# Kernel optimization log

Measured on AMD Instinct MI355X. Metric: run time of the kernel, lower is better.

## Reference

```python
import jax, jax.numpy as jnp
import numpy as np

NUM_ROUTING = 3
EPS = 1e-8


def squash(s, axis=-1):
    # v = ||s||^2/(1+||s||^2) * s/||s||
    sq = jnp.sum(s * s, axis=axis, keepdims=True)
    return sq / (1.0 + sq) * s / (jnp.sqrt(sq) + EPS)


def setup_inputs() -> dict:
    key = jax.random.key(0)
    k1, k2 = jax.random.split(key)
    batch, in_caps, in_dim = 16, 2048, 64
    num_caps, dim_caps = 64, 32
    x = jax.random.normal(k1, (batch, in_caps, in_dim), dtype=jnp.float32)
    # learned transform W[j, d, k]  (torch shape (1,num_caps,1,dim_caps,in_dim) with singletons dropped)
    W = 0.01 * jax.random.normal(k2, (num_caps, dim_caps, in_dim), dtype=jnp.float32)
    return {"x": x, "W": W}


def reference(x, W):
    # u_hat[b,j,i,d] = sum_k W[j,d,k] * x[b,i,k]
    u_hat = jnp.einsum('jdk,bik->bjid', W, x)  # (b, num_caps, in_caps, dim_caps)
    u_hat_d = jax.lax.stop_gradient(u_hat)     # routing uses detached predictions

    b = jnp.zeros(u_hat.shape[:3] + (1,), dtype=u_hat.dtype)  # (b, J, I, 1)
    for _ in range(NUM_ROUTING - 1):
        c = jax.nn.softmax(b, axis=1)                # over output capsules J
        s = jnp.sum(c * u_hat_d, axis=2)             # (b, J, D)
        v = squash(s)
        # agreement uv[b,j,i] = <u_hat_d[b,j,i,:], v[b,j,:]>
        b = b + jnp.einsum('bjid,bjd->bji', u_hat_d, v)[..., None]

    c = jax.nn.softmax(b, axis=1)
    s = jnp.sum(c * u_hat, axis=2)
    return squash(s)  # (b, num_caps, dim_caps)
```

## Files before the change

kernel.cpp:

```cpp
#include <hip/hip_runtime.h>
#include <math.h>


#define BB 16
#define II 2048
#define KK 64
#define JJ 64
#define DD 32
#define ITILE 64
#define NT (II / ITILE)
#define YB 16

typedef float f32x4 __attribute__((ext_vector_type(4)));
typedef short bf16x8 __attribute__((ext_vector_type(8)));

__device__ __forceinline__ unsigned short f2bf(float f) {
    unsigned int u = __float_as_uint(f);
    u += 0x7FFFu + ((u >> 16) & 1u);
    return (unsigned short)(u >> 16);
}

__global__ __launch_bounds__(256) void ybar_kernel(const float* __restrict__ x,
                                                   float* __restrict__ ybarp) {
    const int b = blockIdx.x;
    const int q = blockIdx.y;
    const int tid = threadIdx.x;
    const int kq = tid & 15;
    const int r  = tid >> 4;
    const float4* xp = (const float4*)(x + ((size_t)b * II + (size_t)q * 128) * KK) + kq;
    float4 a = make_float4(0.f, 0.f, 0.f, 0.f);
    #pragma unroll
    for (int n = 0; n < 8; ++n) {
        const float4 v = xp[(size_t)(r + n * 16) * 16];
        a.x += v.x; a.y += v.y; a.z += v.z; a.w += v.w;
    }
    __shared__ float4 sm[16][17];
    sm[r][kq] = a;
    __syncthreads();
    if (tid < 64) {
        const float* smf = (const float*)sm;
        float s = 0.f;
        #pragma unroll
        for (int rr = 0; rr < 16; ++rr) s += smf[rr * 68 + tid];
        ybarp[(b * YB + q) * KK + tid] = s * (1.0f / 64.0f);
    }
}

template <int MODE>
__global__ __launch_bounds__(256) void caps_kernel(const float* __restrict__ W,
                                                   const float* __restrict__ ybarp,
                                                   const float* __restrict__ ypart,
                                                   float* __restrict__ wv,
                                                   float* __restrict__ out) {
    const int b = blockIdx.x;
    const int jq = blockIdx.y;
    const int tid = threadIdx.x;
    const int w = tid >> 6;
    const int lane = tid & 63;
    const int j = jq * 4 + w;

    __shared__ alignas(16) float W_sm[4][DD][68];
    __shared__ alignas(16) float y_sm[4][KK];
    __shared__ float v_sm[4][DD];

    const float* Wp = W + (size_t)j * DD * KK;
    #pragma unroll
    for (int rr = 0; rr < 8; ++rr) {
        const int idx = rr * 64 + lane;
        const int d = idx >> 4, kq = idx & 15;
        *(float4*)&W_sm[w][d][kq * 4] = *(const float4*)(Wp + d * KK + kq * 4);
    }

    if (MODE == 0) {
        const float* yp = ybarp + (size_t)b * YB * KK + lane;
        float a = 0.f;
        #pragma unroll
        for (int t = 0; t < YB; ++t) a += yp[(size_t)t * KK];
        y_sm[w][lane] = a;
    } else {
        const int kq = lane & 15, th = lane >> 4;
        float4 a = make_float4(0.f, 0.f, 0.f, 0.f);
        #pragma unroll
        for (int n = 0; n < 8; ++n) {
            const int t = th + n * 4;
            const float4 v = *(const float4*)(ypart +
                (((size_t)b * NT + t) * JJ + j) * KK + kq * 4);
            a.x += v.x; a.y += v.y; a.z += v.z; a.w += v.w;
        }
        a.x += __shfl_xor(a.x, 16, 64); a.y += __shfl_xor(a.y, 16, 64);
        a.z += __shfl_xor(a.z, 16, 64); a.w += __shfl_xor(a.w, 16, 64);
        a.x += __shfl_xor(a.x, 32, 64); a.y += __shfl_xor(a.y, 32, 64);
        a.z += __shfl_xor(a.z, 32, 64); a.w += __shfl_xor(a.w, 32, 64);
        if (lane < 16) *(float4*)&y_sm[w][kq * 4] = a;
    }

    const int d = lane & 31;
    const int kh = (lane >> 5) * 32;
    float sv = 0.f;
    #pragma unroll
    for (int kq = 0; kq < 8; ++kq) {
        const float4 wr = *(const float4*)&W_sm[w][d][kh + kq * 4];
        const float4 yr = *(const float4*)&y_sm[w][kh + kq * 4];
        sv += wr.x * yr.x + wr.y * yr.y + wr.z * yr.z + wr.w * yr.w;
    }
    sv += __shfl_xor(sv, 32, 64);

    float ps = sv * sv;
    #pragma unroll
    for (int m = 1; m < 32; m <<= 1) ps += __shfl_xor(ps, m, 64);
    const float f = ps / ((1.f + ps) * (sqrtf(ps) + 1e-8f));

    if (MODE == 2) {
        if (lane < DD) out[((size_t)b * JJ + j) * DD + lane] = sv * f;
    } else {
        if (lane < DD) v_sm[w][lane] = sv * f;
        float a = 0.f;
        #pragma unroll
        for (int dd = 0; dd < DD; ++dd) a += W_sm[w][dd][lane] * v_sm[w][dd];
        const size_t idx = ((size_t)b * JJ + j) * KK + lane;
        if (MODE == 1) a += wv[idx];
        wv[idx] = a;
    }
}

#define RPAD 72

__global__ __launch_bounds__(256, 4) void route_kernel(const float* __restrict__ x,
                                                       const float* __restrict__ wv,
                                                       float* __restrict__ ypart) {
    const int b = blockIdx.x;
    const int t = blockIdx.y;
    const int tid = threadIdx.x;
    const int w = tid >> 6;
    const int lr = tid & 15;
    const int lg = (tid >> 4) & 3;

    __shared__ unsigned short x_bf[64][RPAD];
    __shared__ unsigned short xT_bf[64][RPAD];
    __shared__ unsigned short wv_bf[64][RPAD];
    __shared__ unsigned short c_bf[64][RPAD];

    const float4* x4 = (const float4*)(x + ((size_t)b * II + t * ITILE) * KK);
    #pragma unroll
    for (int n = 0; n < 4; ++n) {
        const int idx = tid + n * 256;
        const int i = idx >> 4, kq = idx & 15;
        const float4 v = x4[idx];
        const unsigned short b0 = f2bf(v.x), b1 = f2bf(v.y),
                             b2 = f2bf(v.z), b3 = f2bf(v.w);
        *(unsigned int*)&x_bf[i][kq * 4 + 0] = (unsigned int)b0 | ((unsigned int)b1 << 16);
        *(unsigned int*)&x_bf[i][kq * 4 + 2] = (unsigned int)b2 | ((unsigned int)b3 << 16);
        xT_bf[kq * 4 + 0][i] = b0;
        xT_bf[kq * 4 + 1][i] = b1;
        xT_bf[kq * 4 + 2][i] = b2;
        xT_bf[kq * 4 + 3][i] = b3;
    }
    const float4* wv4 = (const float4*)(wv + (size_t)b * JJ * KK);
    #pragma unroll
    for (int n = 0; n < 4; ++n) {
        const int idx = tid + n * 256;
        const int j = idx >> 4, kq = idx & 15;
        const float4 v = wv4[idx];
        *(unsigned int*)&wv_bf[j][kq * 4 + 0] =
            (unsigned int)f2bf(v.x) | ((unsigned int)f2bf(v.y) << 16);
        *(unsigned int*)&wv_bf[j][kq * 4 + 2] =
            (unsigned int)f2bf(v.z) | ((unsigned int)f2bf(v.w) << 16);
    }
    __syncthreads();

    f32x4 acc[4] = {{0,0,0,0},{0,0,0,0},{0,0,0,0},{0,0,0,0}};
    {
        const bf16x8 a0 = *(const bf16x8*)&x_bf[16 * w + lr][lg * 8];
        const bf16x8 a1 = *(const bf16x8*)&x_bf[16 * w + lr][32 + lg * 8];
        #pragma unroll
        for (int jt = 0; jt < 4; ++jt) {
            const bf16x8 bf0 = *(const bf16x8*)&wv_bf[jt * 16 + lr][lg * 8];
            const bf16x8 bf1 = *(const bf16x8*)&wv_bf[jt * 16 + lr][32 + lg * 8];
            acc[jt] = __builtin_amdgcn_mfma_f32_16x16x32_bf16(a0, bf0, acc[jt], 0, 0, 0);
            acc[jt] = __builtin_amdgcn_mfma_f32_16x16x32_bf16(a1, bf1, acc[jt], 0, 0, 0);
        }
    }

    float c[4][4];
    #pragma unroll
    for (int r = 0; r < 4; ++r) {
        float m = fmaxf(fmaxf(acc[0][r], acc[1][r]), fmaxf(acc[2][r], acc[3][r]));
        m = fmaxf(m, __shfl_xor(m, 1, 64));
        m = fmaxf(m, __shfl_xor(m, 2, 64));
        m = fmaxf(m, __shfl_xor(m, 4, 64));
        m = fmaxf(m, __shfl_xor(m, 8, 64));
        const float e0 = __expf(acc[0][r] - m);
        const float e1 = __expf(acc[1][r] - m);
        const float e2 = __expf(acc[2][r] - m);
        const float e3 = __expf(acc[3][r] - m);
        float s = e0 + e1 + e2 + e3;
        s += __shfl_xor(s, 1, 64);
        s += __shfl_xor(s, 2, 64);
        s += __shfl_xor(s, 4, 64);
        s += __shfl_xor(s, 8, 64);
        const float inv = 1.f / s;
        c[0][r] = e0 * inv; c[1][r] = e1 * inv;
        c[2][r] = e2 * inv; c[3][r] = e3 * inv;
    }

    #pragma unroll
    for (int jt = 0; jt < 4; ++jt) {
        #pragma unroll
        for (int rp = 0; rp < 2; ++rp) {
            const unsigned int pk = (unsigned int)f2bf(c[jt][rp * 2])
                                  | ((unsigned int)f2bf(c[jt][rp * 2 + 1]) << 16);
            *(unsigned int*)&c_bf[jt * 16 + lr][16 * w + lg * 4 + rp * 2] = pk;
        }
    }
    __syncthreads();

    f32x4 acy[4] = {{0,0,0,0},{0,0,0,0},{0,0,0,0},{0,0,0,0}};
    {
        const bf16x8 c0 = *(const bf16x8*)&c_bf[16 * w + lr][lg * 8];
        const bf16x8 c1 = *(const bf16x8*)&c_bf[16 * w + lr][32 + lg * 8];
        #pragma unroll
        for (int kt = 0; kt < 4; ++kt) {
            const bf16x8 xf0 = *(const bf16x8*)&xT_bf[kt * 16 + lr][lg * 8];
            const bf16x8 xf1 = *(const bf16x8*)&xT_bf[kt * 16 + lr][32 + lg * 8];
            acy[kt] = __builtin_amdgcn_mfma_f32_16x16x32_bf16(c0, xf0, acy[kt], 0, 0, 0);
            acy[kt] = __builtin_amdgcn_mfma_f32_16x16x32_bf16(c1, xf1, acy[kt], 0, 0, 0);
        }
    }
    float* yp = ypart + ((size_t)b * NT + t) * JJ * KK;
    #pragma unroll
    for (int kt = 0; kt < 4; ++kt)
        #pragma unroll
        for (int r = 0; r < 4; ++r)
            yp[(16 * w + lg * 4 + r) * KK + kt * 16 + lr] = acy[kt][r];
}

extern "C" void kernel_launch(void* const* d_in, const int* in_sizes, int n_in,
                              void* d_out, int out_size, void* d_ws, size_t ws_size,
                              hipStream_t stream) {
    (void)in_sizes; (void)n_in; (void)out_size; (void)ws_size;
    const float* x = (const float*)d_in[0];
    const float* W = (const float*)d_in[1];
    float* out = (float*)d_out;
    float* ws = (float*)d_ws;

    float* wv    = ws;
    float* ybarp = ws + 65536;
    float* ypart = ws + 65536 + 16384;

    ybar_kernel<<<dim3(BB, YB), 256, 0, stream>>>(x, ybarp);
    caps_kernel<0><<<dim3(BB, 16), 256, 0, stream>>>(W, ybarp, ypart, wv, out);
    route_kernel<<<dim3(BB, NT), 256, 0, stream>>>(x, wv, ypart);
    caps_kernel<1><<<dim3(BB, 16), 256, 0, stream>>>(W, ybarp, ypart, wv, out);
    route_kernel<<<dim3(BB, NT), 256, 0, stream>>>(x, wv, ypart);
    caps_kernel<2><<<dim3(BB, 16), 256, 0, stream>>>(W, ybarp, ypart, wv, out);
}
```

Before: 82.03 us.

## Pre-convert x to bf16 once and store routing partials in bf16

The ybar pass now also writes a bf16 copy of x to workspace, so both route passes read half the bytes and skip the repeated float-to-bf16 conversion. Route partial sums are staged through shared memory and written as bf16 with vectorized stores, and caps_kernel reads and reduces them from bf16. This cuts global memory traffic in the memory-bound passes. The cost is an extra write of x and reduced precision of the partial sums before the final reduction.

```diff
diff --git a/kernel.cpp b/kernel.cpp
--- a/kernel.cpp
+++ b/kernel.cpp
@@ -13,26 +13,37 @@
 
 typedef float f32x4 __attribute__((ext_vector_type(4)));
 typedef short bf16x8 __attribute__((ext_vector_type(8)));
+typedef unsigned short u16x4 __attribute__((ext_vector_type(4)));
+typedef unsigned short u16x8 __attribute__((ext_vector_type(8)));
 
 __device__ __forceinline__ unsigned short f2bf(float f) {
     unsigned int u = __float_as_uint(f);
     u += 0x7FFFu + ((u >> 16) & 1u);
     return (unsigned short)(u >> 16);
 }
+__device__ __forceinline__ float bf2f(unsigned short u) {
+    return __uint_as_float((unsigned int)u << 16);
+}
 
 __global__ __launch_bounds__(256) void ybar_kernel(const float* __restrict__ x,
-                                                   float* __restrict__ ybarp) {
+                                                   float* __restrict__ ybarp,
+                                                   unsigned short* __restrict__ x_bf) {
     const int b = blockIdx.x;
     const int q = blockIdx.y;
     const int tid = threadIdx.x;
     const int kq = tid & 15;
     const int r  = tid >> 4;
-    const float4* xp = (const float4*)(x + ((size_t)b * II + (size_t)q * 128) * KK) + kq;
+    const size_t row0 = (size_t)b * II + (size_t)q * 128;
+    const float4* xp = (const float4*)(x + row0 * KK) + kq;
     float4 a = make_float4(0.f, 0.f, 0.f, 0.f);
     #pragma unroll
     for (int n = 0; n < 8; ++n) {
-        const float4 v = xp[(size_t)(r + n * 16) * 16];
+        const int i = r + n * 16;
+        const float4 v = xp[(size_t)i * 16];
         a.x += v.x; a.y += v.y; a.z += v.z; a.w += v.w;
+        u16x4 bv;
+        bv[0] = f2bf(v.x); bv[1] = f2bf(v.y); bv[2] = f2bf(v.z); bv[3] = f2bf(v.w);
+        *(u16x4*)&x_bf[(row0 + i) * KK + kq * 4] = bv;
     }
     __shared__ float4 sm[16][17];
     sm[r][kq] = a;
@@ -49,7 +60,7 @@
 template <int MODE>
 __global__ __launch_bounds__(256) void caps_kernel(const float* __restrict__ W,
                                                    const float* __restrict__ ybarp,
-                                                   const float* __restrict__ ypart,
+                                                   const unsigned short* __restrict__ ypart_bf,
                                                    float* __restrict__ wv,
                                                    float* __restrict__ out) {
     const int b = blockIdx.x;
@@ -78,20 +89,25 @@
         for (int t = 0; t < YB; ++t) a += yp[(size_t)t * KK];
         y_sm[w][lane] = a;
     } else {
-        const int kq = lane & 15, th = lane >> 4;
-        float4 a = make_float4(0.f, 0.f, 0.f, 0.f);
-        #pragma unroll
-        for (int n = 0; n < 8; ++n) {
-            const int t = th + n * 4;
-            const float4 v = *(const float4*)(ypart +
-                (((size_t)b * NT + t) * JJ + j) * KK + kq * 4);
-            a.x += v.x; a.y += v.y; a.z += v.z; a.w += v.w;
-        }
-        a.x += __shfl_xor(a.x, 16, 64); a.y += __shfl_xor(a.y, 16, 64);
-        a.z += __shfl_xor(a.z, 16, 64); a.w += __shfl_xor(a.w, 16, 64);
-        a.x += __shfl_xor(a.x, 32, 64); a.y += __shfl_xor(a.y, 32, 64);
-        a.z += __shfl_xor(a.z, 32, 64); a.w += __shfl_xor(a.w, 32, 64);
-        if (lane < 16) *(float4*)&y_sm[w][kq * 4] = a;
+        const int kq8 = lane & 7, th = lane >> 3;
+        float a[8] = {0.f, 0.f, 0.f, 0.f, 0.f, 0.f, 0.f, 0.f};
+        #pragma unroll
+        for (int n = 0; n < 4; ++n) {
+            const int tt = th + n * 8;
+            const u16x8 v = *(const u16x8*)(ypart_bf +
+                (((size_t)b * NT + tt) * JJ + j) * KK + kq8 * 8);
+            #pragma unroll
+            for (int m = 0; m < 8; ++m) a[m] += bf2f(v[m]);
+        }
+        #pragma unroll
+        for (int s = 8; s <= 32; s <<= 1) {
+            #pragma unroll
+            for (int m = 0; m < 8; ++m) a[m] += __shfl_xor(a[m], s, 64);
+        }
+        if (th == 0) {
+            #pragma unroll
+            for (int m = 0; m < 8; ++m) y_sm[w][kq8 * 8 + m] = a[m];
+        }
     }
 
     const int d = lane & 31;
@@ -125,9 +141,9 @@
 
 #define RPAD 72
 
-__global__ __launch_bounds__(256, 4) void route_kernel(const float* __restrict__ x,
+__global__ __launch_bounds__(256, 4) void route_kernel(const unsigned short* __restrict__ xg_bf,
                                                        const float* __restrict__ wv,
-                                                       float* __restrict__ ypart) {
+                                                       unsigned short* __restrict__ ypart_bf) {
     const int b = blockIdx.x;
     const int t = blockIdx.y;
     const int tid = threadIdx.x;
@@ -140,20 +156,15 @@
     __shared__ unsigned short wv_bf[64][RPAD];
     __shared__ unsigned short c_bf[64][RPAD];
 
-    const float4* x4 = (const float4*)(x + ((size_t)b * II + t * ITILE) * KK);
-    #pragma unroll
-    for (int n = 0; n < 4; ++n) {
+    const u16x8* xg = (const u16x8*)(xg_bf + ((size_t)b * II + t * ITILE) * KK);
+    #pragma unroll
+    for (int n = 0; n < 2; ++n) {
         const int idx = tid + n * 256;
-        const int i = idx >> 4, kq = idx & 15;
-        const float4 v = x4[idx];
-        const unsigned short b0 = f2bf(v.x), b1 = f2bf(v.y),
-                             b2 = f2bf(v.z), b3 = f2bf(v.w);
-        *(unsigned int*)&x_bf[i][kq * 4 + 0] = (unsigned int)b0 | ((unsigned int)b1 << 16);
-        *(unsigned int*)&x_bf[i][kq * 4 + 2] = (unsigned int)b2 | ((unsigned int)b3 << 16);
-        xT_bf[kq * 4 + 0][i] = b0;
-        xT_bf[kq * 4 + 1][i] = b1;
-        xT_bf[kq * 4 + 2][i] = b2;
-        xT_bf[kq * 4 + 3][i] = b3;
+        const int i = idx >> 3, ch = idx & 7;
+        const u16x8 v = xg[idx];
+        *(u16x8*)&x_bf[i][ch * 8] = v;
+        #pragma unroll
+        for (int m = 0; m < 8; ++m) xT_bf[ch * 8 + m][i] = v[m];
     }
     const float4* wv4 = (const float4*)(wv + (size_t)b * JJ * KK);
     #pragma unroll
@@ -226,12 +237,19 @@
             acy[kt] = __builtin_amdgcn_mfma_f32_16x16x32_bf16(c1, xf1, acy[kt], 0, 0, 0);
         }
     }
-    float* yp = ypart + ((size_t)b * NT + t) * JJ * KK;
     #pragma unroll
     for (int kt = 0; kt < 4; ++kt)
         #pragma unroll
         for (int r = 0; r < 4; ++r)
-            yp[(16 * w + lg * 4 + r) * KK + kt * 16 + lr] = acy[kt][r];
+            wv_bf[16 * w + lg * 4 + r][kt * 16 + lr] = f2bf(acy[kt][r]);
+    __syncthreads();
+    unsigned short* yp = ypart_bf + ((size_t)b * NT + t) * JJ * KK;
+    #pragma unroll
+    for (int n = 0; n < 2; ++n) {
+        const int idx = tid + n * 256;
+        const int row = idx >> 3, ch = idx & 7;
+        *(u16x8*)&yp[row * KK + ch * 8] = *(const u16x8*)&wv_bf[row][ch * 8];
+    }
 }
 
 extern "C" void kernel_launch(void* const* d_in, const int* in_sizes, int n_in,
@@ -245,12 +263,13 @@
 
     float* wv    = ws;
     float* ybarp = ws + 65536;
-    float* ypart = ws + 65536 + 16384;
-
-    ybar_kernel<<<dim3(BB, YB), 256, 0, stream>>>(x, ybarp);
-    caps_kernel<0><<<dim3(BB, 16), 256, 0, stream>>>(W, ybarp, ypart, wv, out);
-    route_kernel<<<dim3(BB, NT), 256, 0, stream>>>(x, wv, ypart);
-    caps_kernel<1><<<dim3(BB, 16), 256, 0, stream>>>(W, ybarp, ypart, wv, out);
-    route_kernel<<<dim3(BB, NT), 256, 0, stream>>>(x, wv, ypart);
-    caps_kernel<2><<<dim3(BB, 16), 256, 0, stream>>>(W, ybarp, ypart, wv, out);
-}
+    unsigned short* x_bf     = (unsigned short*)(ws + 65536 + 16384);
+    unsigned short* ypart_bf = (unsigned short*)(ws + 65536 + 16384 + 1048576);
+
+    ybar_kernel<<<dim3(BB, YB), 256, 0, stream>>>(x, ybarp, x_bf);
+    caps_kernel<0><<<dim3(BB, 16), 256, 0, stream>>>(W, ybarp, ypart_bf, wv, out);
+    route_kernel<<<dim3(BB, NT), 256, 0, stream>>>(x_bf, wv, ypart_bf);
+    caps_kernel<1><<<dim3(BB, 16), 256, 0, stream>>>(W, ybarp, ypart_bf, wv, out);
+    route_kernel<<<dim3(BB, NT), 256, 0, stream>>>(x_bf, wv, ypart_bf);
+    caps_kernel<2><<<dim3(BB, 16), 256, 0, stream>>>(W, ybarp, ypart_bf, wv, out);
+}
```

Measured after the change: 81.14 us. No clear change (-1.1%).
